# Performance work log

Measured on AMD Instinct MI355X. Metric: run time of the kernel, lower is better.

## Reference

```python
import jax, jax.numpy as jnp
import numpy as np

B, DIM_IN, T = 16, 512, 2048
DIM_OUT2 = 512 * 2  # dim_out * 2 (GLU halves it)
K = 3
STYLE = 128
SCALE_CONV = 1.0 / np.sqrt(DIM_IN * K ** 2).astype(np.float32)  # fan_in = dim_in * k^2 (as in source)
SCALE_LIN = 1.0 / np.sqrt(STYLE).astype(np.float32)


def setup_inputs() -> dict:
    key = jax.random.key(0)
    ks = jax.random.split(key, 6)
    x = jax.random.normal(ks[0], (B, DIM_IN, T), dtype=jnp.float32)
    c_src = jax.random.normal(ks[1], (B, STYLE), dtype=jnp.float32)
    c_trg = jax.random.normal(ks[2], (B, STYLE), dtype=jnp.float32)
    # EqualLinear params (lr_mul=1): weight ~ N(0,1), bias filled with bias_init=1
    w_s = jax.random.normal(ks[3], (DIM_IN, STYLE), dtype=jnp.float32)
    b_s = jnp.ones((DIM_IN,), dtype=jnp.float32)
    w_b = jax.random.normal(ks[4], (DIM_IN, STYLE), dtype=jnp.float32)
    b_b = jnp.ones((DIM_IN,), dtype=jnp.float32)
    weight = jax.random.normal(ks[5], (1, DIM_OUT2, DIM_IN, K), dtype=jnp.float32)
    return {"x": x, "c_src": c_src, "c_trg": c_trg,
            "w_s": w_s, "b_s": b_s, "w_b": w_b, "b_b": b_b, "weight": weight}


def reference(x, c_src, c_trg, w_s, b_s, w_b, b_b, weight):
    bsz, cin, t = x.shape
    cout = weight.shape[1]  # dim_out * 2
    k = weight.shape[3]
    # EqualLinear: F.linear(c, w*scale, bias)
    s = (c_trg @ (w_s * SCALE_LIN).T + b_s).reshape(bsz, 1, cin, 1)
    beta = (c_trg @ (w_b * SCALE_LIN).T + b_b).reshape(bsz, 1, cin, 1)
    w = SCALE_CONV * (weight * s + beta)               # [B, Cout, Cin, K]
    demod = jax.lax.rsqrt(jnp.sum(w * w, axis=(2, 3)) + 1e-8)   # [B, Cout]
    demod_mean = jnp.mean(w.reshape(bsz, cout, -1), axis=2)      # [B, Cout]
    w = (w - demod_mean[:, :, None, None]) * demod[:, :, None, None]
    # batch-as-groups conv1d
    w = w.reshape(bsz * cout, cin, k)
    xr = x.reshape(1, bsz * cin, t)
    out = jax.lax.conv_general_dilated(
        xr, w, window_strides=(1,), padding=[(k // 2, k // 2)],
        dimension_numbers=("NCH", "OIH", "NCH"), feature_group_count=bsz)
    out = out.reshape(bsz, cout, -1)
    a, g = jnp.split(out, 2, axis=1)  # GLU on channel dim
    return a * jax.nn.sigmoid(g)
```

## Files before the change

kernel.cpp:

```cpp
#include <hip/hip_runtime.h>
#include <math.h>

typedef __attribute__((ext_vector_type(8))) short short8;
typedef __attribute__((ext_vector_type(8))) unsigned short ushort8;
typedef __attribute__((ext_vector_type(4))) float f32x4;
typedef unsigned short ushortT;

#define NB     16
#define CIN    512
#define TT     2048
#define COUT2  1024
#define NSTYLE 128
#define KKTOT  1536
#define TPAD   2050
#define NKT    24

#define SCALE_LIN  0.088388347648318447f
#define SCALE_CONV 0.014731391274719736f

__device__ __forceinline__ ushortT f2bf(float f) {
  union { float f; unsigned u; } v; v.f = f;
  unsigned r = v.u + 0x7fffu + ((v.u >> 16) & 1u);
  return (ushortT)(r >> 16);
}

__device__ __forceinline__ void gload16(const void* g, void* l) {
  __builtin_amdgcn_global_load_lds(
      (const __attribute__((address_space(1))) void*)g,
      (__attribute__((address_space(3))) void*)l, 16, 0, 0);
}

__global__ void style_kernel(const float* __restrict__ c_trg,
                             const float* __restrict__ w_s, const float* __restrict__ b_s,
                             const float* __restrict__ w_b, const float* __restrict__ b_b,
                             float* __restrict__ s, float* __restrict__ beta,
                             ushortT* __restrict__ xT) {
  int gid = blockIdx.x * 256 + threadIdx.x;
  int b = gid >> 9, ci = gid & 511;
  const float* ct = c_trg + b * NSTYLE;
  const float* ws = w_s + ci * NSTYLE;
  const float* wb = w_b + ci * NSTYLE;
  float as = 0.f, ab = 0.f;
#pragma unroll 8
  for (int j = 0; j < NSTYLE; ++j) {
    float c = ct[j];
    as += c * ws[j];
    ab += c * wb[j];
  }
  s[gid]    = as * SCALE_LIN + b_s[ci];
  beta[gid] = ab * SCALE_LIN + b_b[ci];
  xT[(size_t)b * TPAD * CIN + ci] = 0;
  xT[((size_t)b * TPAD + TPAD - 1) * CIN + ci] = 0;
}

__global__ void xpose_kernel(const float* __restrict__ x, ushortT* __restrict__ xT) {
  int b = blockIdx.z, ct = blockIdx.y, tt = blockIdx.x;
  int t0 = tt * 64, ci0 = ct * 64;
  __shared__ float tile[64][65];
  const float* xB = x + (size_t)b * CIN * TT;
  int rr = threadIdx.x >> 4;
  int c4 = threadIdx.x & 15;
#pragma unroll
  for (int it = 0; it < 4; ++it) {
    int ci = rr + it * 16;
    float4 v = *(const float4*)(xB + (size_t)(ci0 + ci) * TT + t0 + c4 * 4);
    tile[ci][c4 * 4 + 0] = v.x; tile[ci][c4 * 4 + 1] = v.y;
    tile[ci][c4 * 4 + 2] = v.z; tile[ci][c4 * 4 + 3] = v.w;
  }
  __syncthreads();
  ushortT* xTB = xT + (size_t)b * TPAD * CIN;
#pragma unroll
  for (int it = 0; it < 2; ++it) {
    int idx = it * 256 + threadIdx.x;
    int c8 = idx & 7;
    int tl = idx >> 3;
    union { ushort8 v; ushortT u[8]; } o;
#pragma unroll
    for (int j = 0; j < 8; ++j) o.u[j] = f2bf(tile[c8 * 8 + j][tl]);
    *(ushort8*)(xTB + (size_t)(1 + t0 + tl) * CIN + ci0 + c8 * 8) = o.v;
  }
}

__global__ void modw_kernel(const float* __restrict__ weight,
                            const float* __restrict__ s, const float* __restrict__ beta,
                            ushortT* __restrict__ wnorm) {
  int co = blockIdx.x;
  int wv = threadIdx.x >> 6;
  int l  = threadIdx.x & 63;
  const float* wp = weight + (size_t)co * KKTOT + l * 24;
  float v[24];
#pragma unroll
  for (int j = 0; j < 6; ++j) {
    float4 t = *(const float4*)(wp + j * 4);
    v[j * 4 + 0] = t.x; v[j * 4 + 1] = t.y; v[j * 4 + 2] = t.z; v[j * 4 + 3] = t.w;
  }
  int r = ((co & 511) << 1) | (co >> 9);
#pragma unroll
  for (int bi = 0; bi < 4; ++bi) {
    int b = wv * 4 + bi;
    const float* sp = s + b * CIN + l * 8;
    const float* ep = beta + b * CIN + l * 8;
    float4 s0 = *(const float4*)(sp), s1 = *(const float4*)(sp + 4);
    float4 e0 = *(const float4*)(ep), e1 = *(const float4*)(ep + 4);
    float sv[8] = {s0.x, s0.y, s0.z, s0.w, s1.x, s1.y, s1.z, s1.w};
    float ev[8] = {e0.x, e0.y, e0.z, e0.w, e1.x, e1.y, e1.z, e1.w};
    float wm[24];
    float sum = 0.f, sq = 0.f;
#pragma unroll
    for (int c = 0; c < 8; ++c)
#pragma unroll
      for (int k = 0; k < 3; ++k) {
        float val = SCALE_CONV * (v[c * 3 + k] * sv[c] + ev[c]);
        wm[c * 3 + k] = val;
        sum += val; sq += val * val;
      }
#pragma unroll
    for (int off = 32; off; off >>= 1) {
      sum += __shfl_xor(sum, off);
      sq  += __shfl_xor(sq,  off);
    }
    float mean  = sum * (1.0f / 1536.0f);
    float demod = rsqrtf(sq + 1e-8f);
    ushortT* dst = wnorm + ((size_t)b * COUT2 + r) * KKTOT;
#pragma unroll
    for (int k = 0; k < 3; ++k) {
      union { ushort8 v8; ushortT u[8]; } o;
#pragma unroll
      for (int c = 0; c < 8; ++c) o.u[c] = f2bf((wm[c * 3 + k] - mean) * demod);
      *(ushort8*)(dst + k * 512 + l * 8) = o.v8;
    }
  }
}


#define AFRAG(d, s, f) (*(const short8*)(ldsc + ((d) * 4 + (s)) * 16384 + aoff + (f) * 1024))
#define BFRAG(d, s, g) (*(const short8*)(ldsc + ((d) * 4 + (s)) * 16384 + boff + (g) * 1024))

#define RDA(as_, d, s, mh) do {              \
    as_##0 = AFRAG(d, s, (mh) * 4 + 0);      \
    as_##1 = AFRAG(d, s, (mh) * 4 + 1);      \
    as_##2 = AFRAG(d, s, (mh) * 4 + 2);      \
    as_##3 = AFRAG(d, s, (mh) * 4 + 3);      \
  } while (0)

#define RDB(bs_, d, s) do {                  \
    bs_##0 = BFRAG(d, s, 0);                 \
    bs_##1 = BFRAG(d, s, 1);                 \
    bs_##2 = BFRAG(d, s, 2);                 \
    bs_##3 = BFRAG(d, s, 3);                 \
  } while (0)

#define STAGE_A(d, s, kt) do {                                                   \
    int kc_ = (kt) * 64 + (s) * 32;                                              \
    gload16(wB + (size_t)(co0 + r0) * KKTOT + kc_ + jbs8,                        \
            ldsw + ((d) * 4 + (s)) * 8192 + tid * 8);                            \
    gload16(wB + (size_t)(co0 + r0 + 128) * KKTOT + kc_ + jbs8,                  \
            ldsw + ((d) * 4 + (s)) * 8192 + 4096 + tid * 8);                     \
  } while (0)

#define STAGE_B(d, s, kt) do {                                                   \
    int kc_ = (kt) * 64 + (s) * 32;                                              \
    int tap_ = kc_ >> 9; int ci_ = kc_ & 511;                                    \
    gload16(xB + (size_t)(t0 + r0 + tap_) * CIN + ci_ + jbs8,                    \
            ldsw + ((d) * 4 + 2 + (s)) * 8192 + tid * 8);                        \
    gload16(xB + (size_t)(t0 + r0 + 128 + tap_) * CIN + ci_ + jbs8,              \
            ldsw + ((d) * 4 + 2 + (s)) * 8192 + 4096 + tid * 8);                 \
  } while (0)

#define PHASE(mh, au_, bu_, RD_CODE, STAGES, VMN, BAR) do {                      \
    if (BAR) {                                                                   \
      if ((VMN) == 6)      asm volatile("s_waitcnt vmcnt(6)" ::: "memory");      \
      else if ((VMN) == 4) asm volatile("s_waitcnt vmcnt(4)" ::: "memory");      \
      else if ((VMN) == 0) asm volatile("s_waitcnt vmcnt(0)" ::: "memory");      \
      __builtin_amdgcn_s_barrier();                                              \
    }                                                                            \
    STAGES;                                                                      \
    RD_CODE;                                                                     \
    __builtin_amdgcn_sched_barrier(0);     \
    __builtin_amdgcn_s_setprio(1);                                               \
    acc[(mh)*4+0][0] = __builtin_amdgcn_mfma_f32_16x16x32_bf16(au_##0, bu_##0, acc[(mh)*4+0][0], 0, 0, 0); \
    acc[(mh)*4+0][1] = __builtin_amdgcn_mfma_f32_16x16x32_bf16(au_##0, bu_##1, acc[(mh)*4+0][1], 0, 0, 0); \
    acc[(mh)*4+0][2] = __builtin_amdgcn_mfma_f32_16x16x32_bf16(au_##0, bu_##2, acc[(mh)*4+0][2], 0, 0, 0); \
    acc[(mh)*4+0][3] = __builtin_amdgcn_mfma_f32_16x16x32_bf16(au_##0, bu_##3, acc[(mh)*4+0][3], 0, 0, 0); \
    acc[(mh)*4+1][0] = __builtin_amdgcn_mfma_f32_16x16x32_bf16(au_##1, bu_##0, acc[(mh)*4+1][0], 0, 0, 0); \
    acc[(mh)*4+1][1] = __builtin_amdgcn_mfma_f32_16x16x32_bf16(au_##1, bu_##1, acc[(mh)*4+1][1], 0, 0, 0); \
    acc[(mh)*4+1][2] = __builtin_amdgcn_mfma_f32_16x16x32_bf16(au_##1, bu_##2, acc[(mh)*4+1][2], 0, 0, 0); \
    acc[(mh)*4+1][3] = __builtin_amdgcn_mfma_f32_16x16x32_bf16(au_##1, bu_##3, acc[(mh)*4+1][3], 0, 0, 0); \
    acc[(mh)*4+2][0] = __builtin_amdgcn_mfma_f32_16x16x32_bf16(au_##2, bu_##0, acc[(mh)*4+2][0], 0, 0, 0); \
    acc[(mh)*4+2][1] = __builtin_amdgcn_mfma_f32_16x16x32_bf16(au_##2, bu_##1, acc[(mh)*4+2][1], 0, 0, 0); \
    acc[(mh)*4+2][2] = __builtin_amdgcn_mfma_f32_16x16x32_bf16(au_##2, bu_##2, acc[(mh)*4+2][2], 0, 0, 0); \
    acc[(mh)*4+2][3] = __builtin_amdgcn_mfma_f32_16x16x32_bf16(au_##2, bu_##3, acc[(mh)*4+2][3], 0, 0, 0); \
    acc[(mh)*4+3][0] = __builtin_amdgcn_mfma_f32_16x16x32_bf16(au_##3, bu_##0, acc[(mh)*4+3][0], 0, 0, 0); \
    acc[(mh)*4+3][1] = __builtin_amdgcn_mfma_f32_16x16x32_bf16(au_##3, bu_##1, acc[(mh)*4+3][1], 0, 0, 0); \
    acc[(mh)*4+3][2] = __builtin_amdgcn_mfma_f32_16x16x32_bf16(au_##3, bu_##2, acc[(mh)*4+3][2], 0, 0, 0); \
    acc[(mh)*4+3][3] = __builtin_amdgcn_mfma_f32_16x16x32_bf16(au_##3, bu_##3, acc[(mh)*4+3][3], 0, 0, 0); \
    __builtin_amdgcn_s_setprio(0);                                               \
  } while (0)

__global__ __launch_bounds__(512, 2)
void conv_gemm8(const ushortT* __restrict__ wnorm, const ushortT* __restrict__ xT,
                float* __restrict__ out) {
  extern __shared__ ushortT ldsw[];
  const char* ldsc = (const char*)ldsw;

  int orig = blockIdx.x;
  int wgid = (orig & 7) * 64 + (orig >> 3);
  int b  = wgid >> 5;
  int i5 = wgid & 31;
  int mp = i5 >> 4, r2 = i5 & 15;
  int nt = r2 >> 1, mt = mp * 2 + (r2 & 1);
  int co0 = mt * 256, t0 = nt * 256;

  int tid = threadIdx.x;
  int l = tid & 63, w = tid >> 6;
  int wm = w & 1, wn = w >> 1;

  int r0 = tid >> 2;
  int jbs8 = (((tid & 3) ^ ((r0 >> 1) & 3)) << 3);
  int cb = ((l >> 4) ^ ((l >> 1) & 3));
  int aoff = (wm * 128 + (l & 15)) * 64 + cb * 16;
  int boff = 32768 + (wn * 64 + (l & 15)) * 64 + cb * 16;

  const ushortT* wB = wnorm + (size_t)b * COUT2 * KKTOT;
  const ushortT* xB = xT + (size_t)b * TPAD * CIN;

  f32x4 acc[8][4];
#pragma unroll
  for (int i = 0; i < 8; ++i)
#pragma unroll
    for (int j = 0; j < 4; ++j)
      acc[i][j] = (f32x4){0.f, 0.f, 0.f, 0.f};
  short8 ax0 = {}, ax1 = {}, ax2 = {}, ax3 = {};
  short8 ay0 = {}, ay1 = {}, ay2 = {}, ay3 = {};
  short8 bx0 = {}, bx1 = {}, bx2 = {}, bx3 = {};
  short8 by0 = {}, by1 = {}, by2 = {}, by3 = {};

  STAGE_A(0, 0, 0); STAGE_B(0, 0, 0); STAGE_A(0, 1, 0); STAGE_B(0, 1, 0);
  STAGE_B(1, 0, 1); STAGE_A(1, 0, 1); STAGE_B(1, 1, 1);
  asm volatile("s_waitcnt vmcnt(6)" ::: "memory");
  __builtin_amdgcn_s_barrier();
  RDA(ax, 0, 0, 0);
  RDB(bx, 0, 0);

  for (int j = 0; j < 11; ++j) {
    int kt1 = 2 * j + 1;
    int k0n = 2 * j + 2, k1n = 2 * j + 3;
    PHASE(0, ax, bx, { RDA(ay, 0, 0, 1); },                STAGE_A(1, 1, kt1),  6, 1);
    PHASE(1, ay, bx, { RDA(ax, 0, 1, 0); RDB(by, 0, 1); }, STAGE_B(0, 0, k0n), -1, 0);
    PHASE(0, ax, by, { RDA(ay, 0, 1, 1); },                STAGE_A(0, 0, k0n),  6, 1);
    PHASE(1, ay, by, { RDA(ax, 1, 0, 0); RDB(bx, 1, 0); }, STAGE_B(0, 1, k0n), -1, 0);
    PHASE(0, ax, bx, { RDA(ay, 1, 0, 1); },                STAGE_A(0, 1, k0n),  6, 1);
    PHASE(1, ay, bx, { RDA(ax, 1, 1, 0); RDB(by, 1, 1); }, STAGE_B(1, 0, k1n), -1, 0);
    PHASE(0, ax, by, { RDA(ay, 1, 1, 1); },                STAGE_A(1, 0, k1n),  6, 1);
    PHASE(1, ay, by, { RDA(ax, 0, 0, 0); RDB(bx, 0, 0); }, STAGE_B(1, 1, k1n), -1, 0);
  }
  PHASE(0, ax, bx, { RDA(ay, 0, 0, 1); },                STAGE_A(1, 1, 23),  6, 1);
  PHASE(1, ay, bx, { RDA(ax, 0, 1, 0); RDB(by, 0, 1); }, {},                -1, 0);
  PHASE(0, ax, by, { RDA(ay, 0, 1, 1); },                {},                 4, 1);
  PHASE(1, ay, by, { RDA(ax, 1, 0, 0); RDB(bx, 1, 0); }, {},                -1, 0);
  PHASE(0, ax, bx, { RDA(ay, 1, 0, 1); },                {},                 0, 1);
  PHASE(1, ay, bx, { RDA(ax, 1, 1, 0); RDB(by, 1, 1); }, {},                -1, 0);
  PHASE(0, ax, by, { RDA(ay, 1, 1, 1); },                {},                -1, 1);
  PHASE(1, ay, by, { },                                  {},                -1, 0);

#pragma unroll
  for (int f = 0; f < 8; ++f) {
    int cop = co0 + wm * 128 + f * 16 + ((l >> 4) << 2);
    int c = cop >> 1;
    size_t obase = ((size_t)b * (COUT2 / 2) + c) * TT;
#pragma unroll
    for (int g = 0; g < 4; ++g) {
      int t = t0 + wn * 64 + g * 16 + (l & 15);
      f32x4 v = acc[f][g];
      out[obase + t]      = v.x / (1.f + __expf(-v.y));
      out[obase + TT + t] = v.z / (1.f + __expf(-v.w));
    }
  }
}

extern "C" void kernel_launch(void* const* d_in, const int* in_sizes, int n_in,
                              void* d_out, int out_size, void* d_ws, size_t ws_size,
                              hipStream_t stream) {
  const float* x      = (const float*)d_in[0];
  const float* c_trg  = (const float*)d_in[2];
  const float* w_s    = (const float*)d_in[3];
  const float* b_s    = (const float*)d_in[4];
  const float* w_b    = (const float*)d_in[5];
  const float* b_b    = (const float*)d_in[6];
  const float* weight = (const float*)d_in[7];
  float* out = (float*)d_out;

  char* ws = (char*)d_ws;
  float*   s     = (float*)ws;
  float*   beta  = (float*)(ws + 32768);
  ushortT* xT    = (ushortT*)(ws + 65536);
  ushortT* wnorm = (ushortT*)(ws + 65536 + 33587200);

  (void)hipFuncSetAttribute((const void*)conv_gemm8,
                            hipFuncAttributeMaxDynamicSharedMemorySize, 131072);

  style_kernel<<<32, 256, 0, stream>>>(c_trg, w_s, b_s, w_b, b_b, s, beta, xT);
  xpose_kernel<<<dim3(32, 8, 16), 256, 0, stream>>>(x, xT);
  modw_kernel<<<1024, 256, 0, stream>>>(weight, s, beta, wnorm);
  conv_gemm8<<<512, 512, 131072, stream>>>(wnorm, xT, out);
}
```

Measured before the change: 132.6 us.

## Fuse all stages into one cooperative persistent kernel with grid syncs

Replaces the four launches (style, transpose, weight modulation, conv GEMM) with a single cooperative kernel of 256 blocks. The stages are separated by grid-wide syncs, and each block then processes two GEMM tiles in sequence. This removes launch gaps and inter-kernel idle time. In exchange, occupancy drops from two GEMM blocks per CU to one, the GEMM runs as two serialized waves per block, and grid barriers add their own cost.

```diff
diff --git a/kernel.cpp b/kernel.cpp
--- a/kernel.cpp
+++ b/kernel.cpp
@@ -1,5 +1,8 @@
 #include <hip/hip_runtime.h>
+#include <hip/hip_cooperative_groups.h>
 #include <math.h>
+
+namespace cg = cooperative_groups;
 
 typedef __attribute__((ext_vector_type(8))) short short8;
 typedef __attribute__((ext_vector_type(8))) unsigned short ushort8;
@@ -13,7 +16,6 @@
 #define NSTYLE 128
 #define KKTOT  1536
 #define TPAD   2050
-#define NKT    24
 
 #define SCALE_LIN  0.088388347648318447f
 #define SCALE_CONV 0.014731391274719736f
@@ -29,109 +31,6 @@
       (const __attribute__((address_space(1))) void*)g,
       (__attribute__((address_space(3))) void*)l, 16, 0, 0);
 }
-
-__global__ void style_kernel(const float* __restrict__ c_trg,
-                             const float* __restrict__ w_s, const float* __restrict__ b_s,
-                             const float* __restrict__ w_b, const float* __restrict__ b_b,
-                             float* __restrict__ s, float* __restrict__ beta,
-                             ushortT* __restrict__ xT) {
-  int gid = blockIdx.x * 256 + threadIdx.x;
-  int b = gid >> 9, ci = gid & 511;
-  const float* ct = c_trg + b * NSTYLE;
-  const float* ws = w_s + ci * NSTYLE;
-  const float* wb = w_b + ci * NSTYLE;
-  float as = 0.f, ab = 0.f;
-#pragma unroll 8
-  for (int j = 0; j < NSTYLE; ++j) {
-    float c = ct[j];
-    as += c * ws[j];
-    ab += c * wb[j];
-  }
-  s[gid]    = as * SCALE_LIN + b_s[ci];
-  beta[gid] = ab * SCALE_LIN + b_b[ci];
-  xT[(size_t)b * TPAD * CIN + ci] = 0;
-  xT[((size_t)b * TPAD + TPAD - 1) * CIN + ci] = 0;
-}
-
-__global__ void xpose_kernel(const float* __restrict__ x, ushortT* __restrict__ xT) {
-  int b = blockIdx.z, ct = blockIdx.y, tt = blockIdx.x;
-  int t0 = tt * 64, ci0 = ct * 64;
-  __shared__ float tile[64][65];
-  const float* xB = x + (size_t)b * CIN * TT;
-  int rr = threadIdx.x >> 4;
-  int c4 = threadIdx.x & 15;
-#pragma unroll
-  for (int it = 0; it < 4; ++it) {
-    int ci = rr + it * 16;
-    float4 v = *(const float4*)(xB + (size_t)(ci0 + ci) * TT + t0 + c4 * 4);
-    tile[ci][c4 * 4 + 0] = v.x; tile[ci][c4 * 4 + 1] = v.y;
-    tile[ci][c4 * 4 + 2] = v.z; tile[ci][c4 * 4 + 3] = v.w;
-  }
-  __syncthreads();
-  ushortT* xTB = xT + (size_t)b * TPAD * CIN;
-#pragma unroll
-  for (int it = 0; it < 2; ++it) {
-    int idx = it * 256 + threadIdx.x;
-    int c8 = idx & 7;
-    int tl = idx >> 3;
-    union { ushort8 v; ushortT u[8]; } o;
-#pragma unroll
-    for (int j = 0; j < 8; ++j) o.u[j] = f2bf(tile[c8 * 8 + j][tl]);
-    *(ushort8*)(xTB + (size_t)(1 + t0 + tl) * CIN + ci0 + c8 * 8) = o.v;
-  }
-}
-
-__global__ void modw_kernel(const float* __restrict__ weight,
-                            const float* __restrict__ s, const float* __restrict__ beta,
-                            ushortT* __restrict__ wnorm) {
-  int co = blockIdx.x;
-  int wv = threadIdx.x >> 6;
-  int l  = threadIdx.x & 63;
-  const float* wp = weight + (size_t)co * KKTOT + l * 24;
-  float v[24];
-#pragma unroll
-  for (int j = 0; j < 6; ++j) {
-    float4 t = *(const float4*)(wp + j * 4);
-    v[j * 4 + 0] = t.x; v[j * 4 + 1] = t.y; v[j * 4 + 2] = t.z; v[j * 4 + 3] = t.w;
-  }
-  int r = ((co & 511) << 1) | (co >> 9);
-#pragma unroll
-  for (int bi = 0; bi < 4; ++bi) {
-    int b = wv * 4 + bi;
-    const float* sp = s + b * CIN + l * 8;
-    const float* ep = beta + b * CIN + l * 8;
-    float4 s0 = *(const float4*)(sp), s1 = *(const float4*)(sp + 4);
-    float4 e0 = *(const float4*)(ep), e1 = *(const float4*)(ep + 4);
-    float sv[8] = {s0.x, s0.y, s0.z, s0.w, s1.x, s1.y, s1.z, s1.w};
-    float ev[8] = {e0.x, e0.y, e0.z, e0.w, e1.x, e1.y, e1.z, e1.w};
-    float wm[24];
-    float sum = 0.f, sq = 0.f;
-#pragma unroll
-    for (int c = 0; c < 8; ++c)
-#pragma unroll
-      for (int k = 0; k < 3; ++k) {
-        float val = SCALE_CONV * (v[c * 3 + k] * sv[c] + ev[c]);
-        wm[c * 3 + k] = val;
-        sum += val; sq += val * val;
-      }
-#pragma unroll
-    for (int off = 32; off; off >>= 1) {
-      sum += __shfl_xor(sum, off);
-      sq  += __shfl_xor(sq,  off);
-    }
-    float mean  = sum * (1.0f / 1536.0f);
-    float demod = rsqrtf(sq + 1e-8f);
-    ushortT* dst = wnorm + ((size_t)b * COUT2 + r) * KKTOT;
-#pragma unroll
-    for (int k = 0; k < 3; ++k) {
-      union { ushort8 v8; ushortT u[8]; } o;
-#pragma unroll
-      for (int c = 0; c < 8; ++c) o.u[c] = f2bf((wm[c * 3 + k] - mean) * demod);
-      *(ushort8*)(dst + k * 512 + l * 8) = o.v8;
-    }
-  }
-}
-
 
 #define AFRAG(d, s, f) (*(const short8*)(ldsc + ((d) * 4 + (s)) * 16384 + aoff + (f) * 1024))
 #define BFRAG(d, s, g) (*(const short8*)(ldsc + ((d) * 4 + (s)) * 16384 + boff + (g) * 1024))
@@ -176,7 +75,7 @@
     }                                                                            \
     STAGES;                                                                      \
     RD_CODE;                                                                     \
-    __builtin_amdgcn_sched_barrier(0);     \
+    __builtin_amdgcn_sched_barrier(0);                                           \
     __builtin_amdgcn_s_setprio(1);                                               \
     acc[(mh)*4+0][0] = __builtin_amdgcn_mfma_f32_16x16x32_bf16(au_##0, bu_##0, acc[(mh)*4+0][0], 0, 0, 0); \
     acc[(mh)*4+0][1] = __builtin_amdgcn_mfma_f32_16x16x32_bf16(au_##0, bu_##1, acc[(mh)*4+0][1], 0, 0, 0); \
@@ -197,21 +96,17 @@
     __builtin_amdgcn_s_setprio(0);                                               \
   } while (0)
 
-__global__ __launch_bounds__(512, 2)
-void conv_gemm8(const ushortT* __restrict__ wnorm, const ushortT* __restrict__ xT,
-                float* __restrict__ out) {
-  extern __shared__ ushortT ldsw[];
+__device__ __forceinline__ void conv_tile(int wgid, ushortT* ldsw,
+                                          const ushortT* __restrict__ wnorm,
+                                          const ushortT* __restrict__ xT,
+                                          float* __restrict__ out, int tid) {
   const char* ldsc = (const char*)ldsw;
-
-  int orig = blockIdx.x;
-  int wgid = (orig & 7) * 64 + (orig >> 3);
   int b  = wgid >> 5;
   int i5 = wgid & 31;
   int mp = i5 >> 4, r2 = i5 & 15;
   int nt = r2 >> 1, mt = mp * 2 + (r2 & 1);
   int co0 = mt * 256, t0 = nt * 256;
 
-  int tid = threadIdx.x;
   int l = tid & 63, w = tid >> 6;
   int wm = w & 1, wn = w >> 1;
 
@@ -278,6 +173,139 @@
   }
 }
 
+__global__ __launch_bounds__(512, 1)
+void mega(const float* __restrict__ x, const float* __restrict__ c_trg,
+          const float* __restrict__ w_s, const float* __restrict__ b_s,
+          const float* __restrict__ w_b, const float* __restrict__ b_b,
+          const float* __restrict__ weight, float* __restrict__ out,
+          float* __restrict__ s, float* __restrict__ beta,
+          ushortT* __restrict__ xT, ushortT* __restrict__ wnorm) {
+  extern __shared__ ushortT ldsw[];
+  int bid = blockIdx.x;
+  int tid = threadIdx.x;
+
+  if (bid < 16) {
+    int gid = bid * 512 + tid;
+    int b = gid >> 9, ci = gid & 511;
+    const float* ct = c_trg + b * NSTYLE;
+    const float* ws = w_s + ci * NSTYLE;
+    const float* wb = w_b + ci * NSTYLE;
+    float as = 0.f, ab = 0.f;
+#pragma unroll 8
+    for (int j = 0; j < NSTYLE; ++j) {
+      float c = ct[j];
+      as += c * ws[j];
+      ab += c * wb[j];
+    }
+    s[gid]    = as * SCALE_LIN + b_s[ci];
+    beta[gid] = ab * SCALE_LIN + b_b[ci];
+    xT[(size_t)b * TPAD * CIN + ci] = 0;
+    xT[((size_t)b * TPAD + TPAD - 1) * CIN + ci] = 0;
+  }
+
+  {
+    float* tf = (float*)ldsw;
+    int half = tid >> 8;
+    int ltid = tid & 255;
+    float* myTile = tf + half * (64 * 65);
+    int rr = ltid >> 4;
+    int c4 = ltid & 15;
+    for (int it = 0; it < 8; ++it) {
+      int u = bid * 16 + it * 2 + half;
+      int ub = u >> 8, uct = (u >> 5) & 7, utt = u & 31;
+      int t0 = utt * 64, ci0 = uct * 64;
+      const float* xB = x + (size_t)ub * CIN * TT;
+#pragma unroll
+      for (int k = 0; k < 4; ++k) {
+        int ci = rr + k * 16;
+        float4 v = *(const float4*)(xB + (size_t)(ci0 + ci) * TT + t0 + c4 * 4);
+        myTile[ci * 65 + c4 * 4 + 0] = v.x; myTile[ci * 65 + c4 * 4 + 1] = v.y;
+        myTile[ci * 65 + c4 * 4 + 2] = v.z; myTile[ci * 65 + c4 * 4 + 3] = v.w;
+      }
+      __syncthreads();
+      ushortT* xTB = xT + (size_t)ub * TPAD * CIN;
+#pragma unroll
+      for (int it2 = 0; it2 < 2; ++it2) {
+        int idx = it2 * 256 + ltid;
+        int c8 = idx & 7;
+        int tl = idx >> 3;
+        union { ushort8 v8; ushortT u16[8]; } o;
+#pragma unroll
+        for (int j = 0; j < 8; ++j) o.u16[j] = f2bf(myTile[(c8 * 8 + j) * 65 + tl]);
+        *(ushort8*)(xTB + (size_t)(1 + t0 + tl) * CIN + ci0 + c8 * 8) = o.v8;
+      }
+      __syncthreads();
+    }
+  }
+
+  __threadfence();
+  cg::this_grid().sync();
+
+  {
+    int wv = tid >> 6, l = tid & 63;
+    int wv4 = wv & 3;
+    for (int pass = 0; pass < 2; ++pass) {
+      int co = bid * 4 + pass * 2 + (wv >> 2);
+      const float* wp = weight + (size_t)co * KKTOT + l * 24;
+      float v[24];
+#pragma unroll
+      for (int j = 0; j < 6; ++j) {
+        float4 t = *(const float4*)(wp + j * 4);
+        v[j * 4 + 0] = t.x; v[j * 4 + 1] = t.y; v[j * 4 + 2] = t.z; v[j * 4 + 3] = t.w;
+      }
+      int r = ((co & 511) << 1) | (co >> 9);
+#pragma unroll
+      for (int bi = 0; bi < 4; ++bi) {
+        int b = wv4 * 4 + bi;
+        const float* sp = s + b * CIN + l * 8;
+        const float* ep = beta + b * CIN + l * 8;
+        float4 s0 = *(const float4*)(sp), s1 = *(const float4*)(sp + 4);
+        float4 e0 = *(const float4*)(ep), e1 = *(const float4*)(ep + 4);
+        float sv[8] = {s0.x, s0.y, s0.z, s0.w, s1.x, s1.y, s1.z, s1.w};
+        float ev[8] = {e0.x, e0.y, e0.z, e0.w, e1.x, e1.y, e1.z, e1.w};
+        float wm[24];
+        float sum = 0.f, sq = 0.f;
+#pragma unroll
+        for (int c = 0; c < 8; ++c)
+#pragma unroll
+          for (int k = 0; k < 3; ++k) {
+            float val = SCALE_CONV * (v[c * 3 + k] * sv[c] + ev[c]);
+            wm[c * 3 + k] = val;
+            sum += val; sq += val * val;
+          }
+#pragma unroll
+        for (int off = 32; off; off >>= 1) {
+          sum += __shfl_xor(sum, off);
+          sq  += __shfl_xor(sq,  off);
+        }
+        float mean  = sum * (1.0f / 1536.0f);
+        float demod = rsqrtf(sq + 1e-8f);
+        ushortT* dst = wnorm + ((size_t)b * COUT2 + r) * KKTOT;
+#pragma unroll
+        for (int k = 0; k < 3; ++k) {
+          union { ushort8 v8; ushortT u16[8]; } o;
+#pragma unroll
+          for (int c = 0; c < 8; ++c) o.u16[c] = f2bf((wm[c * 3 + k] - mean) * demod);
+          *(ushort8*)(dst + k * 512 + l * 8) = o.v8;
+        }
+      }
+    }
+  }
+
+  __threadfence();
+  cg::this_grid().sync();
+
+  {
+    int orig = bid;
+    int wgid = (orig & 7) * 64 + (orig >> 3);
+    conv_tile(wgid, ldsw, wnorm, xT, out, tid);
+    __syncthreads();
+    orig = bid + 256;
+    wgid = (orig & 7) * 64 + (orig >> 3);
+    conv_tile(wgid, ldsw, wnorm, xT, out, tid);
+  }
+}
+
 extern "C" void kernel_launch(void* const* d_in, const int* in_sizes, int n_in,
                               void* d_out, int out_size, void* d_ws, size_t ws_size,
                               hipStream_t stream) {
@@ -296,11 +324,12 @@
   ushortT* xT    = (ushortT*)(ws + 65536);
   ushortT* wnorm = (ushortT*)(ws + 65536 + 33587200);
 
-  (void)hipFuncSetAttribute((const void*)conv_gemm8,
+  (void)hipFuncSetAttribute((const void*)mega,
                             hipFuncAttributeMaxDynamicSharedMemorySize, 131072);
 
-  style_kernel<<<32, 256, 0, stream>>>(c_trg, w_s, b_s, w_b, b_b, s, beta, xT);
-  xpose_kernel<<<dim3(32, 8, 16), 256, 0, stream>>>(x, xT);
-  modw_kernel<<<1024, 256, 0, stream>>>(weight, s, beta, wnorm);
-  conv_gemm8<<<512, 512, 131072, stream>>>(wnorm, xT, out);
-}
+  void* args[12] = {(void*)&x, (void*)&c_trg, (void*)&w_s, (void*)&b_s,
+                    (void*)&w_b, (void*)&b_b, (void*)&weight, (void*)&out,
+                    (void*)&s, (void*)&beta, (void*)&xT, (void*)&wnorm};
+  (void)hipLaunchCooperativeKernel((void*)mega, dim3(256), dim3(512),
+                                   args, 131072, stream);
+}
```

New measurement: 326.7 us. 146% more time.
